# Kernel optimization log

Hardware: AMD Instinct MI355X
Metric: run time of the kernel (lower is better)

Reference implementation:

```python
import jax, jax.numpy as jnp
import numpy as np

CSIZE = 512
KSIZE = 7
BATCH = 4096


def setup_inputs() -> dict:
    key = jax.random.key(0)
    kx, kw, kb = jax.random.split(key, 3)
    x = jax.random.normal(kx, (BATCH, CSIZE, KSIZE, KSIZE), dtype=jnp.float32)
    # per-channel Conv2d(1,1,ksize) weights: one (ksize,ksize) filter + scalar bias per channel
    fan_in = KSIZE * KSIZE  # PyTorch Conv2d kaiming-uniform bound ~ 1/sqrt(fan_in)
    bound = 1.0 / np.sqrt(fan_in)
    W = jax.random.uniform(kw, (CSIZE, KSIZE, KSIZE), minval=-bound, maxval=bound, dtype=jnp.float32)
    b = jax.random.uniform(kb, (CSIZE,), minval=-bound, maxval=bound, dtype=jnp.float32)
    return {"x": x, "W": W, "b": b}


def reference(x, W, b):
    # Each channel i: Conv2d(1,1,ksize) on a ksize x ksize input -> single scalar,
    # i.e. a weighted sum over the spatial plane plus bias, followed by tanh.
    # Fused across all channels as one contraction: [B,C,H,W] x [C,H,W] -> [B,C]
    s = jnp.einsum("bchw,chw->bc", x, W) + b  # (B, C)
    return jnp.tanh(s)
```

## Files before the change

### kernel.cpp

```cpp
#include <hip/hip_runtime.h>
#include <math.h>


constexpr int K    = 49;
constexpr int ROWS = 256;
constexpr int GRID = 2048;

typedef float f32x4 __attribute__((ext_vector_type(4)));

__global__ __launch_bounds__(256) void WGP_84018150245011_kernel(
    const float* __restrict__ x,
    const float* __restrict__ W,
    const float* __restrict__ bias,
    float* __restrict__ out,
    int n_tiles) {
  __shared__ float xs[ROWS * K];

  const int tid  = threadIdx.x;
  const int wave = tid >> 6;
  const int lane = tid & 63;

  const int c = ((blockIdx.x & 1) << 8) | tid;

  float w[K];
  const float* __restrict__ wr = W + c * K;
#pragma unroll
  for (int k = 0; k < K; ++k) w[k] = wr[k];
  const float bi = bias[c];

  float* myq  = xs + wave * (64 * K);
  f32x4* dst4 = reinterpret_cast<f32x4*>(myq);
  const float* xr = myq + lane * K;

  f32x4 p[12];
  f32x4 ptail;

  auto issue = [&](int g) {
    const f32x4* __restrict__ src4 =
        reinterpret_cast<const f32x4*>(x) + (size_t)g * (ROWS * K / 4) + wave * 784;
#pragma unroll
    for (int j = 0; j < 12; ++j) p[j] = __builtin_nontemporal_load(&src4[lane + j * 64]);
    if (lane < 16) ptail = __builtin_nontemporal_load(&src4[768 + lane]);
  };

  int g = blockIdx.x;
  issue(g);

#pragma unroll 1
  for (;;) {
#pragma unroll
    for (int j = 0; j < 12; ++j) dst4[lane + j * 64] = p[j];
    if (lane < 16) dst4[768 + lane] = ptail;

    const int gn = g + GRID;
    const bool more = (gn < n_tiles);

    if (more) issue(gn);

    float s = bi;
#pragma unroll
    for (int k = 0; k < K; ++k) s = fmaf(xr[k], w[k], s);
    __builtin_nontemporal_store(tanhf(s), &out[(size_t)g * ROWS + tid]);

    if (!more) break;
    g = gn;
  }
}

extern "C" void kernel_launch(void* const* d_in, const int* in_sizes, int n_in,
                              void* d_out, int out_size, void* d_ws, size_t ws_size,
                              hipStream_t stream) {
  const float* x    = (const float*)d_in[0];
  const float* W    = (const float*)d_in[1];
  const float* bias = (const float*)d_in[2];
  float* out        = (float*)d_out;

  const int n_rows  = in_sizes[0] / K;
  const int n_tiles = n_rows / ROWS;

  WGP_84018150245011_kernel<<<GRID, ROWS, 0, stream>>>(x, W, bias, out, n_tiles);
}
```

Baseline: 70.28 us.

## Double-buffer register prefetch to keep two tiles of loads in flight

The single register prefetch buffer becomes two alternating buffers, A and B, so each block has loads for two future tiles outstanding while it computes the current one. The loop is unrolled by two over a fixed iteration count, n_tiles/GRID. This should hide more global-memory latency in a bandwidth-bound kernel. In exchange it uses roughly 52 more VGPRs per thread, which can lower occupancy, and it assumes n_tiles is an even multiple of GRID (true here: 8 tiles per block) and that every block has at least two tiles.

```diff
diff --git a/kernel.cpp b/kernel.cpp
--- a/kernel.cpp
+++ b/kernel.cpp
@@ -32,38 +32,52 @@
   f32x4* dst4 = reinterpret_cast<f32x4*>(myq);
   const float* xr = myq + lane * K;
 
-  f32x4 p[12];
-  f32x4 ptail;
+  f32x4 pA[12], pB[12];
+  f32x4 tailA, tailB;
 
-  auto issue = [&](int g) {
+  auto issueA = [&](int g) {
     const f32x4* __restrict__ src4 =
         reinterpret_cast<const f32x4*>(x) + (size_t)g * (ROWS * K / 4) + wave * 784;
 #pragma unroll
-    for (int j = 0; j < 12; ++j) p[j] = __builtin_nontemporal_load(&src4[lane + j * 64]);
-    if (lane < 16) ptail = __builtin_nontemporal_load(&src4[768 + lane]);
+    for (int j = 0; j < 12; ++j) pA[j] = __builtin_nontemporal_load(&src4[lane + j * 64]);
+    if (lane < 16) tailA = __builtin_nontemporal_load(&src4[768 + lane]);
+  };
+  auto issueB = [&](int g) {
+    const f32x4* __restrict__ src4 =
+        reinterpret_cast<const f32x4*>(x) + (size_t)g * (ROWS * K / 4) + wave * 784;
+#pragma unroll
+    for (int j = 0; j < 12; ++j) pB[j] = __builtin_nontemporal_load(&src4[lane + j * 64]);
+    if (lane < 16) tailB = __builtin_nontemporal_load(&src4[768 + lane]);
   };
 
-  int g = blockIdx.x;
-  issue(g);
-
-#pragma unroll 1
-  for (;;) {
-#pragma unroll
-    for (int j = 0; j < 12; ++j) dst4[lane + j * 64] = p[j];
-    if (lane < 16) dst4[768 + lane] = ptail;
-
-    const int gn = g + GRID;
-    const bool more = (gn < n_tiles);
-
-    if (more) issue(gn);
-
+  auto compute = [&](int g) {
     float s = bi;
 #pragma unroll
     for (int k = 0; k < K; ++k) s = fmaf(xr[k], w[k], s);
     __builtin_nontemporal_store(tanhf(s), &out[(size_t)g * ROWS + tid]);
+  };
 
-    if (!more) break;
-    g = gn;
+  const int iters = n_tiles / GRID;
+  int g = blockIdx.x;
+
+  issueA(g);
+  issueB(g + GRID);
+
+#pragma unroll 1
+  for (int k = 0; k < iters; k += 2) {
+#pragma unroll
+    for (int j = 0; j < 12; ++j) dst4[lane + j * 64] = pA[j];
+    if (lane < 16) dst4[768 + lane] = tailA;
+    if (k + 2 < iters) issueA(g + 2 * GRID);
+    compute(g);
+
+#pragma unroll
+    for (int j = 0; j < 12; ++j) dst4[lane + j * 64] = pB[j];
+    if (lane < 16) dst4[768 + lane] = tailB;
+    if (k + 3 < iters) issueB(g + 3 * GRID);
+    compute(g + GRID);
+
+    g += 2 * GRID;
   }
 }
 
```

After: 70.47 us. About the same (+0.3%).
